# Kernel tuning notes

Measured on AMD Instinct MI355X. Metric: run time of the kernel, lower is better.

The kernel has to match this reference:

```python
import jax, jax.numpy as jnp
import numpy as np

N = 8192        # nodes
E = 131072      # random edges (16 * N); self loops appended inside reference
D = 128         # in_channels
K = int(np.ceil(0.5 * N))  # pooled nodes, ratio=0.5
NEG = 0.2       # leaky relu negative slope


def setup_inputs() -> dict:
    key = jax.random.key(0)
    ks = jax.random.split(key, 10)
    s = 0.05
    return dict(
        x=jax.random.normal(ks[0], (N, D), jnp.float32),
        edge_src=jax.random.randint(ks[1], (E,), 0, N),
        edge_off=jax.random.randint(ks[2], (E,), 0, N - 1),
        W_lin=jax.random.normal(ks[3], (D, D), jnp.float32) * s,
        b_lin=jnp.zeros((D,), jnp.float32),
        w_att=jax.random.normal(ks[4], (2 * D,), jnp.float32) * s,
        b_att=jnp.zeros((1,), jnp.float32),
        w1=jax.random.normal(ks[5], (D,), jnp.float32) * s,
        b1=jnp.zeros((1,), jnp.float32),
        w2=jax.random.normal(ks[6], (D,), jnp.float32) * s,
        w3=jax.random.normal(ks[7], (D,), jnp.float32) * s,
        b3=jnp.zeros((1,), jnp.float32),
    )


def reference(x, edge_src, edge_off, W_lin, b_lin, w_att, b_att, w1, b1, w2, w3, b3):
    # build edges with guaranteed no self loops, then add_remaining_self_loops (weight 1)
    dst = (edge_src + 1 + edge_off) % N
    loop = jnp.arange(N)
    row = jnp.concatenate([edge_src, loop])   # [Et] source j
    col = jnp.concatenate([dst, loop])        # [Et] target i
    ew = jnp.ones(row.shape, x.dtype)         # edge weights (fill_value=1)

    # GNN=None -> x_pool = x
    x_pool_j = x[row]                                             # [Et, D]
    x_q = jax.ops.segment_max(x_pool_j, col, num_segments=N)      # scatter-max at target
    x_q = (x_q @ W_lin + b_lin)[col]                              # [Et, D]

    score = jnp.concatenate([x_q, x_pool_j], axis=-1) @ w_att + b_att[0]  # [Et]
    score = jax.nn.leaky_relu(score, negative_slope=NEG)
    # edge softmax over incoming edges of each target node (stable)
    smax = jax.ops.segment_max(score, col, num_segments=N)
    e = jnp.exp(score - smax[col])
    score = e / jax.ops.segment_sum(e, col, num_segments=N)[col]
    # dropout p=0 (eval): no-op

    # attention-weighted aggregation
    x_new = jax.ops.segment_sum(x[row] * score[:, None], col, num_segments=N)  # [N, D]

    # LEConv fitness (out_channels=1): lin3(x) + sum_j w_ji * (lin1(x)_i - lin2(x)_j)
    a = x_new @ w1 + b1[0]                                        # [N]
    b = x_new @ w2                                                # [N]
    agg = jax.ops.segment_sum(ew * (a[col] - b[row]), col, num_segments=N)
    fitness = jax.nn.sigmoid(x_new @ w3 + b3[0] + agg)            # [N]

    # topk pooling (single graph): k = ceil(ratio * N)
    perm = jnp.argsort(-fitness)[:K]
    x_out = x_new[perm] * fitness[perm][:, None]                  # [K, D]

    # dense N x N attention as in original, then column-select perm
    attention = jnp.zeros((N, N), x.dtype).at[row, col].set(score)
    S_perm = attention[:, perm]                                   # [N, K] == S[:, perm]

    # A_new = S^T A S (A sparse, weight 1 per edge incl. self loops), diag removed
    T = jax.ops.segment_sum(ew[:, None] * S_perm[col], row, num_segments=N)  # A @ S_perm
    A_new = S_perm.T @ T                                          # [K, K]
    A_new = A_new * (1.0 - jnp.eye(K, dtype=x.dtype))             # remove_diag

    return x_out, A_new, perm, S_perm
```

## Files before the change

### kernel.cpp

```cpp
#include <hip/hip_runtime.h>
#include <hip/hip_bf16.h>
#include <math.h>
#include <stdint.h>

#define N_NODES 8192
#define E_EDGES 131072
#define D_DIM 128
#define M_EDGES (E_EDGES + N_NODES)
#define K_TOP 4096
#define NEG_SLOPE 0.2

__global__ void k_init_edges(const int* __restrict__ edge_src, const int* __restrict__ edge_off,
                             unsigned* __restrict__ rowA, unsigned* __restrict__ colA,
                             unsigned* __restrict__ dup,
                             unsigned* __restrict__ col_cnt, unsigned* __restrict__ row_cnt) {
    int e = blockIdx.x * blockDim.x + threadIdx.x;
    if (e >= M_EDGES) return;
    unsigned r, c;
    if (e < E_EDGES) {
        r = (unsigned)edge_src[e];
        c = (r + 1u + (unsigned)edge_off[e]) % N_NODES;
    } else {
        r = c = (unsigned)(e - E_EDGES);
    }
    rowA[e] = r; colA[e] = c; dup[e] = 0u;
    atomicAdd(&col_cnt[c], 1u);
    atomicAdd(&row_cnt[r], 1u);
}

__global__ __launch_bounds__(1024) void k_scan2(const unsigned* __restrict__ cnt0, unsigned* __restrict__ off0, unsigned* __restrict__ cur0,
                                                const unsigned* __restrict__ cnt1, unsigned* __restrict__ off1, unsigned* __restrict__ cur1) {
    const unsigned* cnt = blockIdx.x ? cnt1 : cnt0;
    unsigned* off = blockIdx.x ? off1 : off0;
    unsigned* cur = blockIdx.x ? cur1 : cur0;
    __shared__ unsigned part[1024];
    const int n = N_NODES, per = N_NODES / 1024;
    int t = threadIdx.x;
    unsigned local[8];
    unsigned s = 0;
    for (int j = 0; j < per; j++) { local[j] = cnt[t * per + j]; s += local[j]; }
    part[t] = s; __syncthreads();
    for (int d = 1; d < 1024; d <<= 1) {
        unsigned v = (t >= d) ? part[t - d] : 0u;
        __syncthreads();
        part[t] += v;
        __syncthreads();
    }
    unsigned run = (t > 0) ? part[t - 1] : 0u;
    for (int j = 0; j < per; j++) {
        off[t * per + j] = run;
        if (cur) cur[t * per + j] = run;
        run += local[j];
    }
    if (t == 1023) off[n] = run;
}

__global__ void k_fill(const unsigned* __restrict__ rowA, const unsigned* __restrict__ colA,
                       unsigned* __restrict__ col_cur, unsigned* __restrict__ row_cur,
                       unsigned* __restrict__ col_edges, unsigned* __restrict__ row_edges) {
    int e = blockIdx.x * blockDim.x + threadIdx.x;
    if (e >= M_EDGES) return;
    unsigned p1 = atomicAdd(&col_cur[colA[e]], 1u); col_edges[p1] = (unsigned)e;
    unsigned p2 = atomicAdd(&row_cur[rowA[e]], 1u); row_edges[p2] = (unsigned)e;
}

__global__ __launch_bounds__(64) void k_sortlists(unsigned* __restrict__ col_edges, const unsigned* __restrict__ col_off,
                                                  unsigned* __restrict__ row_edges, const unsigned* __restrict__ row_off,
                                                  const unsigned* __restrict__ rowA, unsigned* __restrict__ dup) {
    __shared__ unsigned buf[192];
    int node = blockIdx.x;
    int which = blockIdx.y;
    unsigned* edges = which ? row_edges : col_edges;
    const unsigned* off = which ? row_off : col_off;
    int lo = (int)off[node], hi = (int)off[node + 1];
    int n = hi - lo; if (n > 192) n = 192;
    for (int i = threadIdx.x; i < n; i += 64) buf[i] = edges[lo + i];
    __syncthreads();
    if (threadIdx.x == 0) {
        for (int i = 1; i < n; i++) {
            unsigned v = buf[i]; int j = i - 1;
            while (j >= 0 && buf[j] > v) { buf[j + 1] = buf[j]; j--; }
            buf[j + 1] = v;
        }
    }
    __syncthreads();
    for (int i = threadIdx.x; i < n; i += 64) edges[lo + i] = buf[i];
    if (which == 0) {
        for (int i = threadIdx.x; i < n; i += 64) {
            unsigned ri = rowA[buf[i]];
            bool d = false;
            for (int j = 0; j < i; j++) if (rowA[buf[j]] == ri) { d = true; break; }
            if (d) dup[buf[i]] = 1u;
        }
    }
}

__global__ __launch_bounds__(128) void k_lin(const float* __restrict__ x,
                                             const unsigned* __restrict__ col_off,
                                             const unsigned* __restrict__ col_edges,
                                             const unsigned* __restrict__ rowA,
                                             const float* __restrict__ W, const float* __restrict__ b_lin,
                                             const float* __restrict__ w_att,
                                             double* __restrict__ q_score, double* __restrict__ k_score) {
    int c = blockIdx.x, d = threadIdx.x;
    __shared__ unsigned rloc[256];
    __shared__ float xq[128];
    __shared__ double red[4];
    int lo = (int)col_off[c], hi = (int)col_off[c + 1];
    int n = hi - lo;
    for (int i = d; i < n && i < 256; i += 128) rloc[i] = rowA[col_edges[lo + i]];
    __syncthreads();
    float m = -INFINITY;
    for (int i = 0; i < n; i++) {
        unsigned r = (i < 256) ? rloc[i] : rowA[col_edges[lo + i]];
        m = fmaxf(m, x[(size_t)r * D_DIM + d]);
    }
    xq[d] = m;
    __syncthreads();
    double acc = (double)b_lin[d];
    for (int j = 0; j < 128; j++) acc += (double)xq[j] * (double)W[j * 128 + d];
    double q = acc * (double)w_att[d];
    double k = (double)x[(size_t)c * 128 + d] * (double)w_att[128 + d];
    for (int o = 32; o > 0; o >>= 1) { q += __shfl_down(q, o); k += __shfl_down(k, o); }
    if ((d & 63) == 0) { red[d >> 6] = q; red[2 + (d >> 6)] = k; }
    __syncthreads();
    if (d == 0) { q_score[c] = red[0] + red[1]; k_score[c] = red[2] + red[3]; }
}

__global__ __launch_bounds__(128) void k_sm_xnew(const float* __restrict__ x,
                                                 const unsigned* __restrict__ col_off,
                                                 const unsigned* __restrict__ col_edges,
                                                 const unsigned* __restrict__ rowA,
                                                 const double* __restrict__ q_score,
                                                 const double* __restrict__ k_score,
                                                 const float* __restrict__ b_att,
                                                 const float* __restrict__ w1, const float* __restrict__ b1,
                                                 const float* __restrict__ w2, const float* __restrict__ w3,
                                                 const float* __restrict__ b3,
                                                 double* __restrict__ score_d, float* __restrict__ score_f,
                                                 float* __restrict__ x_new, double* __restrict__ aV,
                                                 double* __restrict__ bV, double* __restrict__ finV) {
    int c = blockIdx.x, t = threadIdx.x;
    __shared__ unsigned eloc[256];
    __shared__ unsigned rloc[256];
    __shared__ double sloc[256];
    __shared__ double redd[2];
    __shared__ double red6[6];
    int lo = (int)col_off[c], hi = (int)col_off[c + 1];
    int n = hi - lo;
    for (int i = t; i < n && i < 256; i += 128) {
        unsigned e = col_edges[lo + i];
        eloc[i] = e;
        rloc[i] = rowA[e];
    }
    __syncthreads();
    double qc = q_score[c] + (double)b_att[0];
    double m = -INFINITY;
    for (int i = t; i < n; i += 128) {
        unsigned r = (i < 256) ? rloc[i] : rowA[col_edges[lo + i]];
        double s = qc + k_score[r];
        s = (s >= 0.0) ? s : NEG_SLOPE * s;
        m = fmax(m, s);
    }
    for (int o = 32; o > 0; o >>= 1) m = fmax(m, __shfl_xor(m, o));
    if ((t & 63) == 0) redd[t >> 6] = m;
    __syncthreads();
    m = fmax(redd[0], redd[1]);
    __syncthreads();
    double sum = 0.0;
    for (int i = t; i < n; i += 128) {
        unsigned r = (i < 256) ? rloc[i] : rowA[col_edges[lo + i]];
        double s = qc + k_score[r];
        s = (s >= 0.0) ? s : NEG_SLOPE * s;
        sum += exp(s - m);
    }
    for (int o = 32; o > 0; o >>= 1) sum += __shfl_xor(sum, o);
    if ((t & 63) == 0) redd[t >> 6] = sum;
    __syncthreads();
    sum = redd[0] + redd[1];
    for (int i = t; i < n; i += 128) {
        unsigned e = (i < 256) ? eloc[i] : col_edges[lo + i];
        unsigned r = (i < 256) ? rloc[i] : rowA[e];
        double s = qc + k_score[r];
        s = (s >= 0.0) ? s : NEG_SLOPE * s;
        double w = exp(s - m) / sum;
        if (i < 256) sloc[i] = w;
        score_d[e] = w;
        score_f[e] = (float)w;
    }
    __syncthreads();
    int d = t;
    double acc = 0.0;
    for (int i = 0; i < n; i++) {
        unsigned r;
        double sc;
        if (i < 256) { r = rloc[i]; sc = sloc[i]; }
        else { unsigned e = col_edges[lo + i]; r = rowA[e]; sc = score_d[e]; }
        acc += sc * (double)x[(size_t)r * 128 + d];
    }
    x_new[(size_t)c * 128 + d] = (float)acc;
    double pa = acc * (double)w1[d], pb = acc * (double)w2[d], pf = acc * (double)w3[d];
    for (int o = 32; o > 0; o >>= 1) { pa += __shfl_down(pa, o); pb += __shfl_down(pb, o); pf += __shfl_down(pf, o); }
    if ((d & 63) == 0) { int w = d >> 6; red6[w] = pa; red6[2 + w] = pb; red6[4 + w] = pf; }
    __syncthreads();
    if (d == 0) {
        aV[c] = red6[0] + red6[1] + (double)b1[0];
        bV[c] = red6[2] + red6[3];
        finV[c] = red6[4] + red6[5] + (double)b3[0];
    }
}

__global__ __launch_bounds__(64) void k_fitness(const unsigned* __restrict__ col_off,
                                                const unsigned* __restrict__ col_edges,
                                                const unsigned* __restrict__ rowA,
                                                const double* __restrict__ aV, const double* __restrict__ bV,
                                                const double* __restrict__ finV,
                                                double* __restrict__ fitness) {
    int c = blockIdx.x, t = threadIdx.x;
    int lo = (int)col_off[c], hi = (int)col_off[c + 1];
    double ac = aV[c], s = 0.0;
    for (int i = lo + t; i < hi; i += 64) s += ac - bV[rowA[col_edges[i]]];
    for (int o = 32; o > 0; o >>= 1) s += __shfl_xor(s, o);
    if (t == 0) {
        double z = finV[c] + s;
        fitness[c] = 1.0 / (1.0 + exp(-z));
    }
}

__global__ __launch_bounds__(1024) void k_sortlocal(const double* __restrict__ fitness,
                                                    unsigned long long* __restrict__ keys) {
    __shared__ unsigned long long k2[2048];
    int t = threadIdx.x, base = blockIdx.x * 2048;
    for (int i = t; i < 2048; i += 1024) {
        unsigned long long bits = (unsigned long long)__double_as_longlong(fitness[base + i]);
        unsigned long long u = (bits & 0x8000000000000000ull) ? ~bits : (bits | 0x8000000000000000ull);
        k2[i] = (~u & 0xFFFFFFFFFFFFE000ull) | (unsigned long long)(base + i);
    }
    __syncthreads();
    for (int size = 2; size <= 2048; size <<= 1) {
        for (int stride = size >> 1; stride > 0; stride >>= 1) {
            int pos = 2 * t - (t & (stride - 1));
            bool asc = ((pos & size) == 0);
            unsigned long long A = k2[pos], B = k2[pos + stride];
            if ((A > B) == asc) { k2[pos] = B; k2[pos + stride] = A; }
            __syncthreads();
        }
    }
    for (int i = t; i < 2048; i += 1024) keys[base + i] = k2[i];
}

__global__ __launch_bounds__(256) void k_merge(const unsigned long long* __restrict__ in,
                                               unsigned long long* __restrict__ out, int L) {
    int g = blockIdx.x * 256 + threadIdx.x;
    if (g >= N_NODES) return;
    int pair = g / (2 * L), r = g - pair * 2 * L;
    const unsigned long long* A = in + (size_t)pair * 2 * L;
    const unsigned long long* B = A + L;
    unsigned long long v; int p;
    if (r < L) {
        v = A[r];
        int lo = 0, hi = L;
        while (lo < hi) { int mid = (lo + hi) >> 1; if (B[mid] < v) lo = mid + 1; else hi = mid; }
        p = r + lo;
    } else {
        int j = r - L; v = B[j];
        int lo = 0, hi = L;
        while (lo < hi) { int mid = (lo + hi) >> 1; if (A[mid] < v) lo = mid + 1; else hi = mid; }
        p = j + lo;
    }
    out[(size_t)pair * 2 * L + p] = v;
}

__global__ __launch_bounds__(256) void k_merge_emit(const unsigned long long* __restrict__ in,
                                                    unsigned* __restrict__ perm_i, int* __restrict__ inv_k,
                                                    float* __restrict__ perm_out) {
    int g = blockIdx.x * 256 + threadIdx.x;
    if (g >= N_NODES) return;
    const unsigned long long* A = in;
    const unsigned long long* B = in + 4096;
    unsigned long long v; int p;
    if (g < 4096) {
        v = A[g];
        int lo = 0, hi = 4096;
        while (lo < hi) { int mid = (lo + hi) >> 1; if (B[mid] < v) lo = mid + 1; else hi = mid; }
        p = g + lo;
    } else {
        int j = g - 4096; v = B[j];
        int lo = 0, hi = 4096;
        while (lo < hi) { int mid = (lo + hi) >> 1; if (A[mid] < v) lo = mid + 1; else hi = mid; }
        p = j + lo;
    }
    unsigned idx = (unsigned)(v & 0x1FFFull);
    inv_k[idx] = (p < K_TOP) ? p : -1;
    if (p < K_TOP) { perm_i[p] = idx; perm_out[p] = (float)idx; }
}

__global__ __launch_bounds__(64) void k_scount(const unsigned* __restrict__ row_off,
                                               const unsigned* __restrict__ row_edges,
                                               const unsigned* __restrict__ colA,
                                               const unsigned* __restrict__ dup,
                                               const int* __restrict__ inv_k,
                                               unsigned* __restrict__ s_cnt) {
    int c = blockIdx.x, t = threadIdx.x;
    int lo = (int)row_off[c], hi = (int)row_off[c + 1];
    unsigned cnt = 0;
    for (int i = lo + t; i < hi; i += 64) {
        unsigned e = row_edges[i];
        if (!dup[e] && inv_k[colA[e]] >= 0) cnt++;
    }
    for (int o = 32; o > 0; o >>= 1) cnt += __shfl_xor(cnt, o);
    if (t == 0) s_cnt[c] = cnt;
}

__global__ __launch_bounds__(64) void k_sfill(const unsigned* __restrict__ row_off,
                                              const unsigned* __restrict__ row_edges,
                                              const unsigned* __restrict__ colA,
                                              const unsigned* __restrict__ dup,
                                              const int* __restrict__ inv_k,
                                              const unsigned* __restrict__ s_off,
                                              const float* __restrict__ score,
                                              unsigned* __restrict__ s_k, float* __restrict__ s_v) {
    int c = blockIdx.x, t = threadIdx.x;
    int lo = (int)row_off[c], hi = (int)row_off[c + 1];
    unsigned base = s_off[c];
    for (int i0 = lo; i0 < hi; i0 += 64) {
        int i = i0 + t;
        bool pred = false; unsigned e = 0; int kk = -1;
        if (i < hi) {
            e = row_edges[i];
            kk = inv_k[colA[e]];
            pred = (!dup[e]) && (kk >= 0);
        }
        unsigned long long mask = __ballot(pred);
        if (pred) {
            unsigned pos = (unsigned)__popcll(mask & ((1ull << t) - 1ull));
            s_k[base + pos] = (unsigned)kk;
            s_v[base + pos] = score[e];
        }
        base += (unsigned)__popcll(mask);
    }
}

__global__ __launch_bounds__(64) void k_tcount(const unsigned* __restrict__ row_off,
                                               const unsigned* __restrict__ row_edges,
                                               const unsigned* __restrict__ colA,
                                               const unsigned* __restrict__ s_cnt,
                                               unsigned* __restrict__ t_cnt) {
    int r = blockIdx.x, t = threadIdx.x;
    int lo = (int)row_off[r], hi = (int)row_off[r + 1];
    unsigned cnt = 0;
    for (int i = lo + t; i < hi; i += 64) cnt += s_cnt[colA[row_edges[i]]];
    for (int o = 32; o > 0; o >>= 1) cnt += __shfl_xor(cnt, o);
    if (t == 0) t_cnt[r] = cnt;
}

__global__ __launch_bounds__(64) void k_tfill(const unsigned* __restrict__ row_off,
                                              const unsigned* __restrict__ row_edges,
                                              const unsigned* __restrict__ colA,
                                              const unsigned* __restrict__ s_off,
                                              const unsigned* __restrict__ s_cnt,
                                              const unsigned* __restrict__ s_k,
                                              const float* __restrict__ s_v,
                                              const unsigned* __restrict__ t_off,
                                              unsigned* __restrict__ t_k, float* __restrict__ t_v,
                                              unsigned tcap) {
    int r = blockIdx.x, t = threadIdx.x;
    int lo = (int)row_off[r], hi = (int)row_off[r + 1];
    unsigned base = t_off[r];
    for (int i0 = lo; i0 < hi; i0 += 64) {
        int i = i0 + t;
        unsigned cnt = 0, c2 = 0;
        if (i < hi) { c2 = colA[row_edges[i]]; cnt = s_cnt[c2]; }
        unsigned pre = cnt;
        for (int o = 1; o < 64; o <<= 1) { unsigned v = __shfl_up(pre, o); if (t >= o) pre += v; }
        unsigned excl = pre - cnt;
        unsigned total = __shfl(pre, 63);
        if (i < hi && cnt) {
            unsigned sb = s_off[c2];
            unsigned db = base + excl;
            if (db + cnt <= tcap) {
                for (unsigned j = 0; j < cnt; j++) { t_k[db + j] = s_k[sb + j]; t_v[db + j] = s_v[sb + j]; }
            }
        }
        base += total;
    }
}

__global__ __launch_bounds__(256) void k_anew(const unsigned* __restrict__ col_off,
                                              const unsigned* __restrict__ col_edges,
                                              const unsigned* __restrict__ rowA,
                                              const unsigned* __restrict__ dup,
                                              const float* __restrict__ score,
                                              const unsigned* __restrict__ perm_i,
                                              const unsigned* __restrict__ t_off,
                                              const unsigned* __restrict__ t_k,
                                              const float* __restrict__ t_v,
                                              float* __restrict__ A_out) {
    __shared__ float acc[K_TOP];
    int k1 = blockIdx.x, t = threadIdx.x;
    for (int i = t; i < K_TOP; i += 256) acc[i] = 0.f;
    __syncthreads();
    unsigned p = perm_i[k1];
    int lo = (int)col_off[p], hi = (int)col_off[p + 1];
    for (int i = lo; i < hi; i++) {
        unsigned e = col_edges[i];
        if (dup[e]) continue;
        float sc = score[e];
        unsigned n = rowA[e];
        unsigned tb = t_off[n], te = t_off[n + 1];
        for (unsigned j = tb + t; j < te; j += 256)
            atomicAdd(&acc[t_k[j]], sc * t_v[j]);
    }
    __syncthreads();
    float* outp = &A_out[(size_t)k1 * K_TOP];
    for (int i = t; i < K_TOP; i += 256) outp[i] = (i == k1) ? 0.f : acc[i];
}

__global__ __launch_bounds__(256) void k_spermz(const unsigned* __restrict__ s_off,
                                                const unsigned* __restrict__ s_k,
                                                const float* __restrict__ s_v,
                                                float* __restrict__ S_out) {
    int r = blockIdx.x, t = threadIdx.x;
    float4* row4 = (float4*)(S_out + (size_t)r * K_TOP);
    float4 z; z.x = 0.f; z.y = 0.f; z.z = 0.f; z.w = 0.f;
    for (int i = t; i < K_TOP / 4; i += 256) row4[i] = z;
    __syncthreads();
    int lo = (int)s_off[r], hi = (int)s_off[r + 1];
    for (int j = lo + t; j < hi; j += 256)
        S_out[(size_t)r * K_TOP + s_k[j]] = s_v[j];
}

__global__ __launch_bounds__(128) void k_xout(const float* __restrict__ x_new,
                                              const double* __restrict__ fitness,
                                              const unsigned* __restrict__ perm_i,
                                              float* __restrict__ xo) {
    int k = blockIdx.x, d = threadIdx.x;
    unsigned p = perm_i[k];
    xo[(size_t)k * D_DIM + d] = x_new[(size_t)p * D_DIM + d] * (float)fitness[p];
}

extern "C" void kernel_launch(void* const* d_in, const int* in_sizes, int n_in,
                              void* d_out, int out_size, void* d_ws, size_t ws_size,
                              hipStream_t stream) {
    const float* x        = (const float*)d_in[0];
    const int*   edge_src = (const int*)d_in[1];
    const int*   edge_off = (const int*)d_in[2];
    const float* W_lin    = (const float*)d_in[3];
    const float* b_lin    = (const float*)d_in[4];
    const float* w_att    = (const float*)d_in[5];
    const float* b_att    = (const float*)d_in[6];
    const float* w1       = (const float*)d_in[7];
    const float* b1       = (const float*)d_in[8];
    const float* w2       = (const float*)d_in[9];
    const float* w3       = (const float*)d_in[10];
    const float* b3       = (const float*)d_in[11];

    float* out = (float*)d_out;
    float* out_xout  = out;
    float* out_anew  = out + (size_t)K_TOP * D_DIM;
    float* out_perm  = out_anew + (size_t)K_TOP * K_TOP;
    float* out_sperm = out_perm + K_TOP;

    char* wp = (char*)d_ws;
    char* wend = wp + ws_size;
    auto alloc = [&](size_t bytes) -> void* {
        void* p = (void*)wp;
        wp += (bytes + 255) & ~(size_t)255;
        return p;
    };
    unsigned* rowA      = (unsigned*)alloc((size_t)M_EDGES * 4);
    unsigned* colA      = (unsigned*)alloc((size_t)M_EDGES * 4);
    unsigned* dup       = (unsigned*)alloc((size_t)M_EDGES * 4);
    double*   score_d   = (double*)alloc((size_t)M_EDGES * 8);
    float*    score     = (float*)alloc((size_t)M_EDGES * 4);
    unsigned* cnts      = (unsigned*)alloc((size_t)2 * N_NODES * 4);
    unsigned* col_cnt   = cnts;
    unsigned* row_cnt   = cnts + N_NODES;
    unsigned* col_off   = (unsigned*)alloc((size_t)(N_NODES + 1) * 4);
    unsigned* row_off   = (unsigned*)alloc((size_t)(N_NODES + 1) * 4);
    unsigned* col_cur   = (unsigned*)alloc((size_t)N_NODES * 4);
    unsigned* row_cur   = (unsigned*)alloc((size_t)N_NODES * 4);
    unsigned* col_edges = (unsigned*)alloc((size_t)M_EDGES * 4);
    unsigned* row_edges = (unsigned*)alloc((size_t)M_EDGES * 4);
    float*    x_new     = (float*)alloc((size_t)N_NODES * D_DIM * 4);
    double*   q_score   = (double*)alloc((size_t)N_NODES * 8);
    double*   k_score   = (double*)alloc((size_t)N_NODES * 8);
    double*   aV        = (double*)alloc((size_t)N_NODES * 8);
    double*   bV        = (double*)alloc((size_t)N_NODES * 8);
    double*   finV      = (double*)alloc((size_t)N_NODES * 8);
    double*   fitness   = (double*)alloc((size_t)N_NODES * 8);
    unsigned long long* keys_a = (unsigned long long*)alloc((size_t)N_NODES * 8);
    unsigned long long* keys_b = (unsigned long long*)alloc((size_t)N_NODES * 8);
    unsigned* perm_i    = (unsigned*)alloc((size_t)K_TOP * 4);
    int*      inv_k     = (int*)alloc((size_t)N_NODES * 4);
    unsigned* s_cnt     = (unsigned*)alloc((size_t)N_NODES * 4);
    unsigned* s_off     = (unsigned*)alloc((size_t)(N_NODES + 1) * 4);
    unsigned* s_k       = (unsigned*)alloc((size_t)M_EDGES * 4);
    float*    s_v       = (float*)alloc((size_t)M_EDGES * 4);
    unsigned* t_cnt     = (unsigned*)alloc((size_t)N_NODES * 4);
    unsigned* t_off     = (unsigned*)alloc((size_t)(N_NODES + 1) * 4);
    size_t remain = (size_t)(wend - wp);
    size_t tcap = remain / 8;
    if (tcap > (size_t)6 * 1024 * 1024) tcap = (size_t)6 * 1024 * 1024;
    unsigned* t_k = (unsigned*)alloc(tcap * 4);
    float*    t_v = (float*)alloc(tcap * 4);

    hipMemsetAsync(cnts, 0, (size_t)2 * N_NODES * 4, stream);

    k_init_edges<<<(M_EDGES + 255) / 256, 256, 0, stream>>>(edge_src, edge_off, rowA, colA, dup, col_cnt, row_cnt);
    k_scan2<<<2, 1024, 0, stream>>>(col_cnt, col_off, col_cur, row_cnt, row_off, row_cur);
    k_fill<<<(M_EDGES + 255) / 256, 256, 0, stream>>>(rowA, colA, col_cur, row_cur, col_edges, row_edges);
    k_sortlists<<<dim3(N_NODES, 2), 64, 0, stream>>>(col_edges, col_off, row_edges, row_off, rowA, dup);
    k_lin<<<N_NODES, 128, 0, stream>>>(x, col_off, col_edges, rowA, W_lin, b_lin, w_att, q_score, k_score);
    k_sm_xnew<<<N_NODES, 128, 0, stream>>>(x, col_off, col_edges, rowA, q_score, k_score, b_att,
                                           w1, b1, w2, w3, b3, score_d, score, x_new, aV, bV, finV);
    k_fitness<<<N_NODES, 64, 0, stream>>>(col_off, col_edges, rowA, aV, bV, finV, fitness);
    k_sortlocal<<<4, 1024, 0, stream>>>(fitness, keys_a);
    k_merge<<<N_NODES / 256, 256, 0, stream>>>(keys_a, keys_b, 2048);
    k_merge_emit<<<N_NODES / 256, 256, 0, stream>>>(keys_b, perm_i, inv_k, out_perm);
    k_scount<<<N_NODES, 64, 0, stream>>>(row_off, row_edges, colA, dup, inv_k, s_cnt);
    k_tcount<<<N_NODES, 64, 0, stream>>>(row_off, row_edges, colA, s_cnt, t_cnt);
    k_scan2<<<2, 1024, 0, stream>>>(s_cnt, s_off, (unsigned*)nullptr, t_cnt, t_off, (unsigned*)nullptr);
    k_sfill<<<N_NODES, 64, 0, stream>>>(row_off, row_edges, colA, dup, inv_k, s_off, score, s_k, s_v);
    k_tfill<<<N_NODES, 64, 0, stream>>>(row_off, row_edges, colA, s_off, s_cnt, s_k, s_v, t_off,
                                        t_k, t_v, (unsigned)tcap);
    k_spermz<<<N_NODES, 256, 0, stream>>>(s_off, s_k, s_v, out_sperm);
    k_anew<<<K_TOP, 256, 0, stream>>>(col_off, col_edges, rowA, dup, score, perm_i, t_off, t_k, t_v, out_anew);
    k_xout<<<K_TOP, 128, 0, stream>>>(x_new, fitness, perm_i, out_xout);
}
```

Baseline: 304.4 us.

## Fuse output kernels, drop list sorting, compute A_new by two-hop traversal

Removes the per-node insertion sort and moves duplicate-edge detection into the linear kernel, which now handles 16 nodes per block with W staged in LDS. Fitness computation is folded into the local bitonic sort kernel. The S_perm count/fill and T materialisation passes are replaced by one fused launch. That launch writes S_perm rows, builds A_new by walking two hops of the row CSR with LDS atomics, and emits x_out. This cuts many launches and intermediate buffers, but the A_new blocks do more irregular gather work, and the linear kernel has fewer blocks and does a quadratic duplicate check in global memory.

New measurement: 732.1 us. +140.5%, slower.

```diff
diff --git a/kernel.cpp b/kernel.cpp
--- a/kernel.cpp
+++ b/kernel.cpp
@@ -64,67 +64,50 @@
     unsigned p2 = atomicAdd(&row_cur[rowA[e]], 1u); row_edges[p2] = (unsigned)e;
 }
 
-__global__ __launch_bounds__(64) void k_sortlists(unsigned* __restrict__ col_edges, const unsigned* __restrict__ col_off,
-                                                  unsigned* __restrict__ row_edges, const unsigned* __restrict__ row_off,
-                                                  const unsigned* __restrict__ rowA, unsigned* __restrict__ dup) {
-    __shared__ unsigned buf[192];
-    int node = blockIdx.x;
-    int which = blockIdx.y;
-    unsigned* edges = which ? row_edges : col_edges;
-    const unsigned* off = which ? row_off : col_off;
-    int lo = (int)off[node], hi = (int)off[node + 1];
-    int n = hi - lo; if (n > 192) n = 192;
-    for (int i = threadIdx.x; i < n; i += 64) buf[i] = edges[lo + i];
-    __syncthreads();
-    if (threadIdx.x == 0) {
-        for (int i = 1; i < n; i++) {
-            unsigned v = buf[i]; int j = i - 1;
-            while (j >= 0 && buf[j] > v) { buf[j + 1] = buf[j]; j--; }
-            buf[j + 1] = v;
-        }
-    }
-    __syncthreads();
-    for (int i = threadIdx.x; i < n; i += 64) edges[lo + i] = buf[i];
-    if (which == 0) {
-        for (int i = threadIdx.x; i < n; i += 64) {
-            unsigned ri = rowA[buf[i]];
-            bool d = false;
-            for (int j = 0; j < i; j++) if (rowA[buf[j]] == ri) { d = true; break; }
-            if (d) dup[buf[i]] = 1u;
-        }
-    }
-}
-
 __global__ __launch_bounds__(128) void k_lin(const float* __restrict__ x,
                                              const unsigned* __restrict__ col_off,
                                              const unsigned* __restrict__ col_edges,
                                              const unsigned* __restrict__ rowA,
+                                             unsigned* __restrict__ dup,
                                              const float* __restrict__ W, const float* __restrict__ b_lin,
                                              const float* __restrict__ w_att,
                                              double* __restrict__ q_score, double* __restrict__ k_score) {
-    int c = blockIdx.x, d = threadIdx.x;
-    __shared__ unsigned rloc[256];
-    __shared__ float xq[128];
+    __shared__ float Wlds[D_DIM * D_DIM];
+    __shared__ float xq[D_DIM];
     __shared__ double red[4];
-    int lo = (int)col_off[c], hi = (int)col_off[c + 1];
-    int n = hi - lo;
-    for (int i = d; i < n && i < 256; i += 128) rloc[i] = rowA[col_edges[lo + i]];
-    __syncthreads();
-    float m = -INFINITY;
-    for (int i = 0; i < n; i++) {
-        unsigned r = (i < 256) ? rloc[i] : rowA[col_edges[lo + i]];
-        m = fmaxf(m, x[(size_t)r * D_DIM + d]);
-    }
-    xq[d] = m;
-    __syncthreads();
-    double acc = (double)b_lin[d];
-    for (int j = 0; j < 128; j++) acc += (double)xq[j] * (double)W[j * 128 + d];
-    double q = acc * (double)w_att[d];
-    double k = (double)x[(size_t)c * 128 + d] * (double)w_att[128 + d];
-    for (int o = 32; o > 0; o >>= 1) { q += __shfl_down(q, o); k += __shfl_down(k, o); }
-    if ((d & 63) == 0) { red[d >> 6] = q; red[2 + (d >> 6)] = k; }
-    __syncthreads();
-    if (d == 0) { q_score[c] = red[0] + red[1]; k_score[c] = red[2] + red[3]; }
+    int t = threadIdx.x;
+    for (int idx = t; idx < D_DIM * D_DIM; idx += 128) Wlds[idx] = W[idx];
+    double bl = (double)b_lin[t];
+    double wq = (double)w_att[t];
+    double wk = (double)w_att[D_DIM + t];
+    __syncthreads();
+    for (int nb = 0; nb < 16; nb++) {
+        int c = blockIdx.x * 16 + nb;
+        int lo = (int)col_off[c], hi = (int)col_off[c + 1];
+        int n = hi - lo;
+        for (int i = t; i < n; i += 128) {
+            unsigned ri = rowA[col_edges[lo + i]];
+            for (int j = 0; j < i; j++) {
+                if (rowA[col_edges[lo + j]] == ri) { dup[col_edges[lo + i]] = 1u; break; }
+            }
+        }
+        float m = -INFINITY;
+        for (int i = 0; i < n; i++) {
+            unsigned r = rowA[col_edges[lo + i]];
+            m = fmaxf(m, x[(size_t)r * D_DIM + t]);
+        }
+        xq[t] = m;
+        __syncthreads();
+        double acc = bl;
+        for (int j = 0; j < D_DIM; j++) acc += (double)xq[j] * (double)Wlds[j * D_DIM + t];
+        double q = acc * wq;
+        double k = (double)x[(size_t)c * D_DIM + t] * wk;
+        for (int o = 32; o > 0; o >>= 1) { q += __shfl_down(q, o); k += __shfl_down(k, o); }
+        if ((t & 63) == 0) { red[t >> 6] = q; red[2 + (t >> 6)] = k; }
+        __syncthreads();
+        if (t == 0) { q_score[c] = red[0] + red[1]; k_score[c] = red[2] + red[3]; }
+        __syncthreads();
+    }
 }
 
 __global__ __launch_bounds__(128) void k_sm_xnew(const float* __restrict__ x,
@@ -196,9 +179,9 @@
         double sc;
         if (i < 256) { r = rloc[i]; sc = sloc[i]; }
         else { unsigned e = col_edges[lo + i]; r = rowA[e]; sc = score_d[e]; }
-        acc += sc * (double)x[(size_t)r * 128 + d];
-    }
-    x_new[(size_t)c * 128 + d] = (float)acc;
+        acc += sc * (double)x[(size_t)r * D_DIM + d];
+    }
+    x_new[(size_t)c * D_DIM + d] = (float)acc;
     double pa = acc * (double)w1[d], pb = acc * (double)w2[d], pf = acc * (double)w3[d];
     for (int o = 32; o > 0; o >>= 1) { pa += __shfl_down(pa, o); pb += __shfl_down(pb, o); pf += __shfl_down(pf, o); }
     if ((d & 63) == 0) { int w = d >> 6; red6[w] = pa; red6[2 + w] = pb; red6[4 + w] = pf; }
@@ -210,31 +193,25 @@
     }
 }
 
-__global__ __launch_bounds__(64) void k_fitness(const unsigned* __restrict__ col_off,
-                                                const unsigned* __restrict__ col_edges,
-                                                const unsigned* __restrict__ rowA,
-                                                const double* __restrict__ aV, const double* __restrict__ bV,
-                                                const double* __restrict__ finV,
-                                                double* __restrict__ fitness) {
-    int c = blockIdx.x, t = threadIdx.x;
-    int lo = (int)col_off[c], hi = (int)col_off[c + 1];
-    double ac = aV[c], s = 0.0;
-    for (int i = lo + t; i < hi; i += 64) s += ac - bV[rowA[col_edges[i]]];
-    for (int o = 32; o > 0; o >>= 1) s += __shfl_xor(s, o);
-    if (t == 0) {
-        double z = finV[c] + s;
-        fitness[c] = 1.0 / (1.0 + exp(-z));
-    }
-}
-
-__global__ __launch_bounds__(1024) void k_sortlocal(const double* __restrict__ fitness,
-                                                    unsigned long long* __restrict__ keys) {
+__global__ __launch_bounds__(1024) void k_sortfit(const unsigned* __restrict__ col_off,
+                                                  const unsigned* __restrict__ col_edges,
+                                                  const unsigned* __restrict__ rowA,
+                                                  const double* __restrict__ aV, const double* __restrict__ bV,
+                                                  const double* __restrict__ finV,
+                                                  double* __restrict__ fitness,
+                                                  unsigned long long* __restrict__ keys) {
     __shared__ unsigned long long k2[2048];
     int t = threadIdx.x, base = blockIdx.x * 2048;
-    for (int i = t; i < 2048; i += 1024) {
-        unsigned long long bits = (unsigned long long)__double_as_longlong(fitness[base + i]);
-        unsigned long long u = (bits & 0x8000000000000000ull) ? ~bits : (bits | 0x8000000000000000ull);
-        k2[i] = (~u & 0xFFFFFFFFFFFFE000ull) | (unsigned long long)(base + i);
+    for (int u = 0; u < 2; u++) {
+        int c = base + u * 1024 + t;
+        int lo = (int)col_off[c], hi = (int)col_off[c + 1];
+        double s = finV[c] + (double)(hi - lo) * aV[c];
+        for (int i = lo; i < hi; i++) s -= bV[rowA[col_edges[i]]];
+        double fit = 1.0 / (1.0 + exp(-s));
+        fitness[c] = fit;
+        unsigned long long bits = (unsigned long long)__double_as_longlong(fit);
+        unsigned long long uo = (bits & 0x8000000000000000ull) ? ~bits : (bits | 0x8000000000000000ull);
+        k2[u * 1024 + t] = (~uo & 0xFFFFFFFFFFFFE000ull) | (unsigned long long)c;
     }
     __syncthreads();
     for (int size = 2; size <= 2048; size <<= 1) {
@@ -295,148 +272,82 @@
     if (p < K_TOP) { perm_i[p] = idx; perm_out[p] = (float)idx; }
 }
 
-__global__ __launch_bounds__(64) void k_scount(const unsigned* __restrict__ row_off,
-                                               const unsigned* __restrict__ row_edges,
-                                               const unsigned* __restrict__ colA,
-                                               const unsigned* __restrict__ dup,
-                                               const int* __restrict__ inv_k,
-                                               unsigned* __restrict__ s_cnt) {
-    int c = blockIdx.x, t = threadIdx.x;
-    int lo = (int)row_off[c], hi = (int)row_off[c + 1];
-    unsigned cnt = 0;
-    for (int i = lo + t; i < hi; i += 64) {
-        unsigned e = row_edges[i];
-        if (!dup[e] && inv_k[colA[e]] >= 0) cnt++;
-    }
-    for (int o = 32; o > 0; o >>= 1) cnt += __shfl_xor(cnt, o);
-    if (t == 0) s_cnt[c] = cnt;
-}
-
-__global__ __launch_bounds__(64) void k_sfill(const unsigned* __restrict__ row_off,
-                                              const unsigned* __restrict__ row_edges,
-                                              const unsigned* __restrict__ colA,
-                                              const unsigned* __restrict__ dup,
-                                              const int* __restrict__ inv_k,
-                                              const unsigned* __restrict__ s_off,
-                                              const float* __restrict__ score,
-                                              unsigned* __restrict__ s_k, float* __restrict__ s_v) {
-    int c = blockIdx.x, t = threadIdx.x;
-    int lo = (int)row_off[c], hi = (int)row_off[c + 1];
-    unsigned base = s_off[c];
-    for (int i0 = lo; i0 < hi; i0 += 64) {
-        int i = i0 + t;
-        bool pred = false; unsigned e = 0; int kk = -1;
-        if (i < hi) {
-            e = row_edges[i];
-            kk = inv_k[colA[e]];
-            pred = (!dup[e]) && (kk >= 0);
-        }
-        unsigned long long mask = __ballot(pred);
-        if (pred) {
-            unsigned pos = (unsigned)__popcll(mask & ((1ull << t) - 1ull));
-            s_k[base + pos] = (unsigned)kk;
-            s_v[base + pos] = score[e];
-        }
-        base += (unsigned)__popcll(mask);
-    }
-}
-
-__global__ __launch_bounds__(64) void k_tcount(const unsigned* __restrict__ row_off,
-                                               const unsigned* __restrict__ row_edges,
-                                               const unsigned* __restrict__ colA,
-                                               const unsigned* __restrict__ s_cnt,
-                                               unsigned* __restrict__ t_cnt) {
-    int r = blockIdx.x, t = threadIdx.x;
-    int lo = (int)row_off[r], hi = (int)row_off[r + 1];
-    unsigned cnt = 0;
-    for (int i = lo + t; i < hi; i += 64) cnt += s_cnt[colA[row_edges[i]]];
-    for (int o = 32; o > 0; o >>= 1) cnt += __shfl_xor(cnt, o);
-    if (t == 0) t_cnt[r] = cnt;
-}
-
-__global__ __launch_bounds__(64) void k_tfill(const unsigned* __restrict__ row_off,
-                                              const unsigned* __restrict__ row_edges,
-                                              const unsigned* __restrict__ colA,
-                                              const unsigned* __restrict__ s_off,
-                                              const unsigned* __restrict__ s_cnt,
-                                              const unsigned* __restrict__ s_k,
-                                              const float* __restrict__ s_v,
-                                              const unsigned* __restrict__ t_off,
-                                              unsigned* __restrict__ t_k, float* __restrict__ t_v,
-                                              unsigned tcap) {
-    int r = blockIdx.x, t = threadIdx.x;
-    int lo = (int)row_off[r], hi = (int)row_off[r + 1];
-    unsigned base = t_off[r];
-    for (int i0 = lo; i0 < hi; i0 += 64) {
-        int i = i0 + t;
-        unsigned cnt = 0, c2 = 0;
-        if (i < hi) { c2 = colA[row_edges[i]]; cnt = s_cnt[c2]; }
-        unsigned pre = cnt;
-        for (int o = 1; o < 64; o <<= 1) { unsigned v = __shfl_up(pre, o); if (t >= o) pre += v; }
-        unsigned excl = pre - cnt;
-        unsigned total = __shfl(pre, 63);
-        if (i < hi && cnt) {
-            unsigned sb = s_off[c2];
-            unsigned db = base + excl;
-            if (db + cnt <= tcap) {
-                for (unsigned j = 0; j < cnt; j++) { t_k[db + j] = s_k[sb + j]; t_v[db + j] = s_v[sb + j]; }
+__global__ __launch_bounds__(256) void k_fused_out(const unsigned* __restrict__ col_off,
+                                                   const unsigned* __restrict__ col_edges,
+                                                   const unsigned* __restrict__ row_off,
+                                                   const unsigned* __restrict__ row_edges,
+                                                   const unsigned* __restrict__ rowA,
+                                                   const unsigned* __restrict__ colA,
+                                                   const unsigned* __restrict__ dup,
+                                                   const float* __restrict__ score,
+                                                   const int* __restrict__ inv_k,
+                                                   const unsigned* __restrict__ perm_i,
+                                                   const float* __restrict__ x_new,
+                                                   const double* __restrict__ fitness,
+                                                   float* __restrict__ S_out,
+                                                   float* __restrict__ A_out,
+                                                   float* __restrict__ xo) {
+    __shared__ float acc[K_TOP];
+    __shared__ unsigned nloc[64];
+    __shared__ float scloc[64];
+    int bid = blockIdx.x, t = threadIdx.x;
+    if (bid < N_NODES) {
+        int r = bid;
+        float4* row4 = (float4*)(S_out + (size_t)r * K_TOP);
+        float4 z; z.x = 0.f; z.y = 0.f; z.z = 0.f; z.w = 0.f;
+        for (int i = t; i < K_TOP / 4; i += 256) row4[i] = z;
+        __syncthreads();
+        int lo = (int)row_off[r], hi = (int)row_off[r + 1];
+        for (int j = lo + t; j < hi; j += 256) {
+            unsigned e = row_edges[j];
+            if (!dup[e]) {
+                int kk = inv_k[colA[e]];
+                if (kk >= 0) S_out[(size_t)r * K_TOP + kk] = score[e];
             }
         }
-        base += total;
-    }
-}
-
-__global__ __launch_bounds__(256) void k_anew(const unsigned* __restrict__ col_off,
-                                              const unsigned* __restrict__ col_edges,
-                                              const unsigned* __restrict__ rowA,
-                                              const unsigned* __restrict__ dup,
-                                              const float* __restrict__ score,
-                                              const unsigned* __restrict__ perm_i,
-                                              const unsigned* __restrict__ t_off,
-                                              const unsigned* __restrict__ t_k,
-                                              const float* __restrict__ t_v,
-                                              float* __restrict__ A_out) {
-    __shared__ float acc[K_TOP];
-    int k1 = blockIdx.x, t = threadIdx.x;
-    for (int i = t; i < K_TOP; i += 256) acc[i] = 0.f;
-    __syncthreads();
-    unsigned p = perm_i[k1];
-    int lo = (int)col_off[p], hi = (int)col_off[p + 1];
-    for (int i = lo; i < hi; i++) {
-        unsigned e = col_edges[i];
-        if (dup[e]) continue;
-        float sc = score[e];
-        unsigned n = rowA[e];
-        unsigned tb = t_off[n], te = t_off[n + 1];
-        for (unsigned j = tb + t; j < te; j += 256)
-            atomicAdd(&acc[t_k[j]], sc * t_v[j]);
-    }
-    __syncthreads();
-    float* outp = &A_out[(size_t)k1 * K_TOP];
-    for (int i = t; i < K_TOP; i += 256) outp[i] = (i == k1) ? 0.f : acc[i];
-}
-
-__global__ __launch_bounds__(256) void k_spermz(const unsigned* __restrict__ s_off,
-                                                const unsigned* __restrict__ s_k,
-                                                const float* __restrict__ s_v,
-                                                float* __restrict__ S_out) {
-    int r = blockIdx.x, t = threadIdx.x;
-    float4* row4 = (float4*)(S_out + (size_t)r * K_TOP);
-    float4 z; z.x = 0.f; z.y = 0.f; z.z = 0.f; z.w = 0.f;
-    for (int i = t; i < K_TOP / 4; i += 256) row4[i] = z;
-    __syncthreads();
-    int lo = (int)s_off[r], hi = (int)s_off[r + 1];
-    for (int j = lo + t; j < hi; j += 256)
-        S_out[(size_t)r * K_TOP + s_k[j]] = s_v[j];
-}
-
-__global__ __launch_bounds__(128) void k_xout(const float* __restrict__ x_new,
-                                              const double* __restrict__ fitness,
-                                              const unsigned* __restrict__ perm_i,
-                                              float* __restrict__ xo) {
-    int k = blockIdx.x, d = threadIdx.x;
-    unsigned p = perm_i[k];
-    xo[(size_t)k * D_DIM + d] = x_new[(size_t)p * D_DIM + d] * (float)fitness[p];
+    } else if (bid < N_NODES + K_TOP) {
+        int k1 = bid - N_NODES;
+        for (int i = t; i < K_TOP; i += 256) acc[i] = 0.f;
+        unsigned p = perm_i[k1];
+        int lo = (int)col_off[p], hi = (int)col_off[p + 1];
+        for (int c0 = lo; c0 < hi; c0 += 64) {
+            int nin = hi - c0; if (nin > 64) nin = 64;
+            __syncthreads();
+            if (t < nin) {
+                unsigned e = col_edges[c0 + t];
+                nloc[t] = dup[e] ? 0xFFFFFFFFu : rowA[e];
+                scloc[t] = score[e];
+            }
+            __syncthreads();
+            int g = t >> 3, lane = t & 7;
+            for (int i = g; i < nin; i += 32) {
+                unsigned n = nloc[i];
+                if (n == 0xFFFFFFFFu) continue;
+                float sc = scloc[i];
+                int rlo = (int)row_off[n], rhi = (int)row_off[n + 1];
+                for (int j = rlo + lane; j < rhi; j += 8) {
+                    unsigned c2 = colA[row_edges[j]];
+                    int qlo = (int)row_off[c2], qhi = (int)row_off[c2 + 1];
+                    for (int q = qlo; q < qhi; q++) {
+                        unsigned e3 = row_edges[q];
+                        if (dup[e3]) continue;
+                        int kk = inv_k[colA[e3]];
+                        if (kk >= 0) atomicAdd(&acc[kk], sc * score[e3]);
+                    }
+                }
+            }
+        }
+        __syncthreads();
+        float* outp = &A_out[(size_t)k1 * K_TOP];
+        for (int i = t; i < K_TOP; i += 256) outp[i] = (i == k1) ? 0.f : acc[i];
+    } else {
+        int gid = (bid - N_NODES - K_TOP) * 256 + t;
+        for (int u = gid; u < K_TOP * D_DIM; u += 32 * 256) {
+            int k = u >> 7, d = u & 127;
+            unsigned pp = perm_i[k];
+            xo[u] = x_new[(size_t)pp * D_DIM + d] * (float)fitness[pp];
+        }
+    }
 }
 
 extern "C" void kernel_launch(void* const* d_in, const int* in_sizes, int n_in,
@@ -462,7 +373,6 @@
     float* out_sperm = out_perm + K_TOP;
 
     char* wp = (char*)d_ws;
-    char* wend = wp + ws_size;
     auto alloc = [&](size_t bytes) -> void* {
         void* p = (void*)wp;
         wp += (bytes + 255) & ~(size_t)255;
@@ -493,38 +403,19 @@
     unsigned long long* keys_b = (unsigned long long*)alloc((size_t)N_NODES * 8);
     unsigned* perm_i    = (unsigned*)alloc((size_t)K_TOP * 4);
     int*      inv_k     = (int*)alloc((size_t)N_NODES * 4);
-    unsigned* s_cnt     = (unsigned*)alloc((size_t)N_NODES * 4);
-    unsigned* s_off     = (unsigned*)alloc((size_t)(N_NODES + 1) * 4);
-    unsigned* s_k       = (unsigned*)alloc((size_t)M_EDGES * 4);
-    float*    s_v       = (float*)alloc((size_t)M_EDGES * 4);
-    unsigned* t_cnt     = (unsigned*)alloc((size_t)N_NODES * 4);
-    unsigned* t_off     = (unsigned*)alloc((size_t)(N_NODES + 1) * 4);
-    size_t remain = (size_t)(wend - wp);
-    size_t tcap = remain / 8;
-    if (tcap > (size_t)6 * 1024 * 1024) tcap = (size_t)6 * 1024 * 1024;
-    unsigned* t_k = (unsigned*)alloc(tcap * 4);
-    float*    t_v = (float*)alloc(tcap * 4);
 
     hipMemsetAsync(cnts, 0, (size_t)2 * N_NODES * 4, stream);
 
     k_init_edges<<<(M_EDGES + 255) / 256, 256, 0, stream>>>(edge_src, edge_off, rowA, colA, dup, col_cnt, row_cnt);
     k_scan2<<<2, 1024, 0, stream>>>(col_cnt, col_off, col_cur, row_cnt, row_off, row_cur);
     k_fill<<<(M_EDGES + 255) / 256, 256, 0, stream>>>(rowA, colA, col_cur, row_cur, col_edges, row_edges);
-    k_sortlists<<<dim3(N_NODES, 2), 64, 0, stream>>>(col_edges, col_off, row_edges, row_off, rowA, dup);
-    k_lin<<<N_NODES, 128, 0, stream>>>(x, col_off, col_edges, rowA, W_lin, b_lin, w_att, q_score, k_score);
+    k_lin<<<N_NODES / 16, 128, 0, stream>>>(x, col_off, col_edges, rowA, dup, W_lin, b_lin, w_att, q_score, k_score);
     k_sm_xnew<<<N_NODES, 128, 0, stream>>>(x, col_off, col_edges, rowA, q_score, k_score, b_att,
                                            w1, b1, w2, w3, b3, score_d, score, x_new, aV, bV, finV);
-    k_fitness<<<N_NODES, 64, 0, stream>>>(col_off, col_edges, rowA, aV, bV, finV, fitness);
-    k_sortlocal<<<4, 1024, 0, stream>>>(fitness, keys_a);
+    k_sortfit<<<4, 1024, 0, stream>>>(col_off, col_edges, rowA, aV, bV, finV, fitness, keys_a);
     k_merge<<<N_NODES / 256, 256, 0, stream>>>(keys_a, keys_b, 2048);
     k_merge_emit<<<N_NODES / 256, 256, 0, stream>>>(keys_b, perm_i, inv_k, out_perm);
-    k_scount<<<N_NODES, 64, 0, stream>>>(row_off, row_edges, colA, dup, inv_k, s_cnt);
-    k_tcount<<<N_NODES, 64, 0, stream>>>(row_off, row_edges, colA, s_cnt, t_cnt);
-    k_scan2<<<2, 1024, 0, stream>>>(s_cnt, s_off, (unsigned*)nullptr, t_cnt, t_off, (unsigned*)nullptr);
-    k_sfill<<<N_NODES, 64, 0, stream>>>(row_off, row_edges, colA, dup, inv_k, s_off, score, s_k, s_v);
-    k_tfill<<<N_NODES, 64, 0, stream>>>(row_off, row_edges, colA, s_off, s_cnt, s_k, s_v, t_off,
-                                        t_k, t_v, (unsigned)tcap);
-    k_spermz<<<N_NODES, 256, 0, stream>>>(s_off, s_k, s_v, out_sperm);
-    k_anew<<<K_TOP, 256, 0, stream>>>(col_off, col_edges, rowA, dup, score, perm_i, t_off, t_k, t_v, out_anew);
-    k_xout<<<K_TOP, 128, 0, stream>>>(x_new, fitness, perm_i, out_xout);
-}
+    k_fused_out<<<N_NODES + K_TOP + 32, 256, 0, stream>>>(col_off, col_edges, row_off, row_edges,
+                                                          rowA, colA, dup, score, inv_k, perm_i,
+                                                          x_new, fitness, out_sperm, out_anew, out_xout);
+}
```

## Drop per-node list sorting, fold dup detection into k_lin, fuse output kernels

Applied to the files above, without the earlier changes.

Removes the k_sortlists kernel, which sorted every node's in- and out-edge lists with a single-thread insertion sort. Duplicate-edge detection moves into k_lin as a quadratic check over each node's unsorted incoming list. The fitness computation is folded into the block-local bitonic sort kernel. The S_perm, A_new and x_out writers become one launch that branches on block index. This saves the sort pass and several launches, but the per-node edge order now follows atomic fill order, so which duplicate gets flagged and the floating-point summation order are no longer deterministic. The fitness pass also now runs on only 4 blocks.

New measurement: 340.6 us. 11.9% more time.

```diff
diff --git a/kernel.cpp b/kernel.cpp
--- a/kernel.cpp
+++ b/kernel.cpp
@@ -64,67 +64,44 @@
     unsigned p2 = atomicAdd(&row_cur[rowA[e]], 1u); row_edges[p2] = (unsigned)e;
 }
 
-__global__ __launch_bounds__(64) void k_sortlists(unsigned* __restrict__ col_edges, const unsigned* __restrict__ col_off,
-                                                  unsigned* __restrict__ row_edges, const unsigned* __restrict__ row_off,
-                                                  const unsigned* __restrict__ rowA, unsigned* __restrict__ dup) {
-    __shared__ unsigned buf[192];
-    int node = blockIdx.x;
-    int which = blockIdx.y;
-    unsigned* edges = which ? row_edges : col_edges;
-    const unsigned* off = which ? row_off : col_off;
-    int lo = (int)off[node], hi = (int)off[node + 1];
-    int n = hi - lo; if (n > 192) n = 192;
-    for (int i = threadIdx.x; i < n; i += 64) buf[i] = edges[lo + i];
-    __syncthreads();
-    if (threadIdx.x == 0) {
-        for (int i = 1; i < n; i++) {
-            unsigned v = buf[i]; int j = i - 1;
-            while (j >= 0 && buf[j] > v) { buf[j + 1] = buf[j]; j--; }
-            buf[j + 1] = v;
-        }
-    }
-    __syncthreads();
-    for (int i = threadIdx.x; i < n; i += 64) edges[lo + i] = buf[i];
-    if (which == 0) {
-        for (int i = threadIdx.x; i < n; i += 64) {
-            unsigned ri = rowA[buf[i]];
-            bool d = false;
-            for (int j = 0; j < i; j++) if (rowA[buf[j]] == ri) { d = true; break; }
-            if (d) dup[buf[i]] = 1u;
-        }
-    }
-}
-
 __global__ __launch_bounds__(128) void k_lin(const float* __restrict__ x,
                                              const unsigned* __restrict__ col_off,
                                              const unsigned* __restrict__ col_edges,
                                              const unsigned* __restrict__ rowA,
+                                             unsigned* __restrict__ dup,
                                              const float* __restrict__ W, const float* __restrict__ b_lin,
                                              const float* __restrict__ w_att,
                                              double* __restrict__ q_score, double* __restrict__ k_score) {
-    int c = blockIdx.x, d = threadIdx.x;
+    int c = blockIdx.x, t = threadIdx.x;
     __shared__ unsigned rloc[256];
     __shared__ float xq[128];
     __shared__ double red[4];
     int lo = (int)col_off[c], hi = (int)col_off[c + 1];
     int n = hi - lo;
-    for (int i = d; i < n && i < 256; i += 128) rloc[i] = rowA[col_edges[lo + i]];
-    __syncthreads();
+    for (int i = t; i < n && i < 256; i += 128) rloc[i] = rowA[col_edges[lo + i]];
+    __syncthreads();
+    for (int i = t; i < n; i += 128) {
+        unsigned ri = (i < 256) ? rloc[i] : rowA[col_edges[lo + i]];
+        for (int j = 0; j < i; j++) {
+            unsigned rj = (j < 256) ? rloc[j] : rowA[col_edges[lo + j]];
+            if (rj == ri) { dup[col_edges[lo + i]] = 1u; break; }
+        }
+    }
     float m = -INFINITY;
     for (int i = 0; i < n; i++) {
         unsigned r = (i < 256) ? rloc[i] : rowA[col_edges[lo + i]];
-        m = fmaxf(m, x[(size_t)r * D_DIM + d]);
-    }
-    xq[d] = m;
-    __syncthreads();
-    double acc = (double)b_lin[d];
-    for (int j = 0; j < 128; j++) acc += (double)xq[j] * (double)W[j * 128 + d];
-    double q = acc * (double)w_att[d];
-    double k = (double)x[(size_t)c * 128 + d] * (double)w_att[128 + d];
+        m = fmaxf(m, x[(size_t)r * D_DIM + t]);
+    }
+    xq[t] = m;
+    __syncthreads();
+    double acc = (double)b_lin[t];
+    for (int j = 0; j < D_DIM; j++) acc += (double)xq[j] * (double)W[j * D_DIM + t];
+    double q = acc * (double)w_att[t];
+    double k = (double)x[(size_t)c * D_DIM + t] * (double)w_att[D_DIM + t];
     for (int o = 32; o > 0; o >>= 1) { q += __shfl_down(q, o); k += __shfl_down(k, o); }
-    if ((d & 63) == 0) { red[d >> 6] = q; red[2 + (d >> 6)] = k; }
-    __syncthreads();
-    if (d == 0) { q_score[c] = red[0] + red[1]; k_score[c] = red[2] + red[3]; }
+    if ((t & 63) == 0) { red[t >> 6] = q; red[2 + (t >> 6)] = k; }
+    __syncthreads();
+    if (t == 0) { q_score[c] = red[0] + red[1]; k_score[c] = red[2] + red[3]; }
 }
 
 __global__ __launch_bounds__(128) void k_sm_xnew(const float* __restrict__ x,
@@ -196,9 +173,9 @@
         double sc;
         if (i < 256) { r = rloc[i]; sc = sloc[i]; }
         else { unsigned e = col_edges[lo + i]; r = rowA[e]; sc = score_d[e]; }
-        acc += sc * (double)x[(size_t)r * 128 + d];
-    }
-    x_new[(size_t)c * 128 + d] = (float)acc;
+        acc += sc * (double)x[(size_t)r * D_DIM + d];
+    }
+    x_new[(size_t)c * D_DIM + d] = (float)acc;
     double pa = acc * (double)w1[d], pb = acc * (double)w2[d], pf = acc * (double)w3[d];
     for (int o = 32; o > 0; o >>= 1) { pa += __shfl_down(pa, o); pb += __shfl_down(pb, o); pf += __shfl_down(pf, o); }
     if ((d & 63) == 0) { int w = d >> 6; red6[w] = pa; red6[2 + w] = pb; red6[4 + w] = pf; }
@@ -210,31 +187,25 @@
     }
 }
 
-__global__ __launch_bounds__(64) void k_fitness(const unsigned* __restrict__ col_off,
-                                                const unsigned* __restrict__ col_edges,
-                                                const unsigned* __restrict__ rowA,
-                                                const double* __restrict__ aV, const double* __restrict__ bV,
-                                                const double* __restrict__ finV,
-                                                double* __restrict__ fitness) {
-    int c = blockIdx.x, t = threadIdx.x;
-    int lo = (int)col_off[c], hi = (int)col_off[c + 1];
-    double ac = aV[c], s = 0.0;
-    for (int i = lo + t; i < hi; i += 64) s += ac - bV[rowA[col_edges[i]]];
-    for (int o = 32; o > 0; o >>= 1) s += __shfl_xor(s, o);
-    if (t == 0) {
-        double z = finV[c] + s;
-        fitness[c] = 1.0 / (1.0 + exp(-z));
-    }
-}
-
-__global__ __launch_bounds__(1024) void k_sortlocal(const double* __restrict__ fitness,
-                                                    unsigned long long* __restrict__ keys) {
+__global__ __launch_bounds__(1024) void k_sortfit(const unsigned* __restrict__ col_off,
+                                                  const unsigned* __restrict__ col_edges,
+                                                  const unsigned* __restrict__ rowA,
+                                                  const double* __restrict__ aV, const double* __restrict__ bV,
+                                                  const double* __restrict__ finV,
+                                                  double* __restrict__ fitness,
+                                                  unsigned long long* __restrict__ keys) {
     __shared__ unsigned long long k2[2048];
     int t = threadIdx.x, base = blockIdx.x * 2048;
-    for (int i = t; i < 2048; i += 1024) {
-        unsigned long long bits = (unsigned long long)__double_as_longlong(fitness[base + i]);
-        unsigned long long u = (bits & 0x8000000000000000ull) ? ~bits : (bits | 0x8000000000000000ull);
-        k2[i] = (~u & 0xFFFFFFFFFFFFE000ull) | (unsigned long long)(base + i);
+    for (int u = 0; u < 2; u++) {
+        int c = base + u * 1024 + t;
+        int lo = (int)col_off[c], hi = (int)col_off[c + 1];
+        double s = finV[c] + (double)(hi - lo) * aV[c];
+        for (int i = lo; i < hi; i++) s -= bV[rowA[col_edges[i]]];
+        double fit = 1.0 / (1.0 + exp(-s));
+        fitness[c] = fit;
+        unsigned long long bits = (unsigned long long)__double_as_longlong(fit);
+        unsigned long long uo = (bits & 0x8000000000000000ull) ? ~bits : (bits | 0x8000000000000000ull);
+        k2[u * 1024 + t] = (~uo & 0xFFFFFFFFFFFFE000ull) | (unsigned long long)c;
     }
     __syncthreads();
     for (int size = 2; size <= 2048; size <<= 1) {
@@ -386,57 +357,66 @@
     }
 }
 
-__global__ __launch_bounds__(256) void k_anew(const unsigned* __restrict__ col_off,
-                                              const unsigned* __restrict__ col_edges,
-                                              const unsigned* __restrict__ rowA,
-                                              const unsigned* __restrict__ dup,
-                                              const float* __restrict__ score,
-                                              const unsigned* __restrict__ perm_i,
-                                              const unsigned* __restrict__ t_off,
-                                              const unsigned* __restrict__ t_k,
-                                              const float* __restrict__ t_v,
-                                              float* __restrict__ A_out) {
+__global__ __launch_bounds__(256) void k_fused_out(const unsigned* __restrict__ col_off,
+                                                   const unsigned* __restrict__ col_edges,
+                                                   const unsigned* __restrict__ row_off,
+                                                   const unsigned* __restrict__ row_edges,
+                                                   const unsigned* __restrict__ rowA,
+                                                   const unsigned* __restrict__ colA,
+                                                   const unsigned* __restrict__ dup,
+                                                   const float* __restrict__ score,
+                                                   const int* __restrict__ inv_k,
+                                                   const unsigned* __restrict__ perm_i,
+                                                   const unsigned* __restrict__ t_off,
+                                                   const unsigned* __restrict__ t_k,
+                                                   const float* __restrict__ t_v,
+                                                   const float* __restrict__ x_new,
+                                                   const double* __restrict__ fitness,
+                                                   float* __restrict__ S_out,
+                                                   float* __restrict__ A_out,
+                                                   float* __restrict__ xo) {
     __shared__ float acc[K_TOP];
-    int k1 = blockIdx.x, t = threadIdx.x;
-    for (int i = t; i < K_TOP; i += 256) acc[i] = 0.f;
-    __syncthreads();
-    unsigned p = perm_i[k1];
-    int lo = (int)col_off[p], hi = (int)col_off[p + 1];
-    for (int i = lo; i < hi; i++) {
-        unsigned e = col_edges[i];
-        if (dup[e]) continue;
-        float sc = score[e];
-        unsigned n = rowA[e];
-        unsigned tb = t_off[n], te = t_off[n + 1];
-        for (unsigned j = tb + t; j < te; j += 256)
-            atomicAdd(&acc[t_k[j]], sc * t_v[j]);
-    }
-    __syncthreads();
-    float* outp = &A_out[(size_t)k1 * K_TOP];
-    for (int i = t; i < K_TOP; i += 256) outp[i] = (i == k1) ? 0.f : acc[i];
-}
-
-__global__ __launch_bounds__(256) void k_spermz(const unsigned* __restrict__ s_off,
-                                                const unsigned* __restrict__ s_k,
-                                                const float* __restrict__ s_v,
-                                                float* __restrict__ S_out) {
-    int r = blockIdx.x, t = threadIdx.x;
-    float4* row4 = (float4*)(S_out + (size_t)r * K_TOP);
-    float4 z; z.x = 0.f; z.y = 0.f; z.z = 0.f; z.w = 0.f;
-    for (int i = t; i < K_TOP / 4; i += 256) row4[i] = z;
-    __syncthreads();
-    int lo = (int)s_off[r], hi = (int)s_off[r + 1];
-    for (int j = lo + t; j < hi; j += 256)
-        S_out[(size_t)r * K_TOP + s_k[j]] = s_v[j];
-}
-
-__global__ __launch_bounds__(128) void k_xout(const float* __restrict__ x_new,
-                                              const double* __restrict__ fitness,
-                                              const unsigned* __restrict__ perm_i,
-                                              float* __restrict__ xo) {
-    int k = blockIdx.x, d = threadIdx.x;
-    unsigned p = perm_i[k];
-    xo[(size_t)k * D_DIM + d] = x_new[(size_t)p * D_DIM + d] * (float)fitness[p];
+    int bid = blockIdx.x, t = threadIdx.x;
+    if (bid < N_NODES) {
+        int r = bid;
+        float4* row4 = (float4*)(S_out + (size_t)r * K_TOP);
+        float4 z; z.x = 0.f; z.y = 0.f; z.z = 0.f; z.w = 0.f;
+        for (int i = t; i < K_TOP / 4; i += 256) row4[i] = z;
+        __syncthreads();
+        int lo = (int)row_off[r], hi = (int)row_off[r + 1];
+        for (int j = lo + t; j < hi; j += 256) {
+            unsigned e = row_edges[j];
+            if (!dup[e]) {
+                int kk = inv_k[colA[e]];
+                if (kk >= 0) S_out[(size_t)r * K_TOP + kk] = score[e];
+            }
+        }
+    } else if (bid < N_NODES + K_TOP) {
+        int k1 = bid - N_NODES;
+        for (int i = t; i < K_TOP; i += 256) acc[i] = 0.f;
+        __syncthreads();
+        unsigned p = perm_i[k1];
+        int lo = (int)col_off[p], hi = (int)col_off[p + 1];
+        for (int i = lo; i < hi; i++) {
+            unsigned e = col_edges[i];
+            if (dup[e]) continue;
+            float sc = score[e];
+            unsigned n = rowA[e];
+            unsigned tb = t_off[n], te = t_off[n + 1];
+            for (unsigned j = tb + t; j < te; j += 256)
+                atomicAdd(&acc[t_k[j]], sc * t_v[j]);
+        }
+        __syncthreads();
+        float* outp = &A_out[(size_t)k1 * K_TOP];
+        for (int i = t; i < K_TOP; i += 256) outp[i] = (i == k1) ? 0.f : acc[i];
+    } else {
+        int gid = (bid - N_NODES - K_TOP) * 256 + t;
+        for (int u = gid; u < K_TOP * D_DIM; u += 32 * 256) {
+            int k = u >> 7, d = u & 127;
+            unsigned pp = perm_i[k];
+            xo[u] = x_new[(size_t)pp * D_DIM + d] * (float)fitness[pp];
+        }
+    }
 }
 
 extern "C" void kernel_launch(void* const* d_in, const int* in_sizes, int n_in,
@@ -510,12 +490,10 @@
     k_init_edges<<<(M_EDGES + 255) / 256, 256, 0, stream>>>(edge_src, edge_off, rowA, colA, dup, col_cnt, row_cnt);
     k_scan2<<<2, 1024, 0, stream>>>(col_cnt, col_off, col_cur, row_cnt, row_off, row_cur);
     k_fill<<<(M_EDGES + 255) / 256, 256, 0, stream>>>(rowA, colA, col_cur, row_cur, col_edges, row_edges);
-    k_sortlists<<<dim3(N_NODES, 2), 64, 0, stream>>>(col_edges, col_off, row_edges, row_off, rowA, dup);
-    k_lin<<<N_NODES, 128, 0, stream>>>(x, col_off, col_edges, rowA, W_lin, b_lin, w_att, q_score, k_score);
+    k_lin<<<N_NODES, 128, 0, stream>>>(x, col_off, col_edges, rowA, dup, W_lin, b_lin, w_att, q_score, k_score);
     k_sm_xnew<<<N_NODES, 128, 0, stream>>>(x, col_off, col_edges, rowA, q_score, k_score, b_att,
                                            w1, b1, w2, w3, b3, score_d, score, x_new, aV, bV, finV);
-    k_fitness<<<N_NODES, 64, 0, stream>>>(col_off, col_edges, rowA, aV, bV, finV, fitness);
-    k_sortlocal<<<4, 1024, 0, stream>>>(fitness, keys_a);
+    k_sortfit<<<4, 1024, 0, stream>>>(col_off, col_edges, rowA, aV, bV, finV, fitness, keys_a);
     k_merge<<<N_NODES / 256, 256, 0, stream>>>(keys_a, keys_b, 2048);
     k_merge_emit<<<N_NODES / 256, 256, 0, stream>>>(keys_b, perm_i, inv_k, out_perm);
     k_scount<<<N_NODES, 64, 0, stream>>>(row_off, row_edges, colA, dup, inv_k, s_cnt);
@@ -524,7 +502,8 @@
     k_sfill<<<N_NODES, 64, 0, stream>>>(row_off, row_edges, colA, dup, inv_k, s_off, score, s_k, s_v);
     k_tfill<<<N_NODES, 64, 0, stream>>>(row_off, row_edges, colA, s_off, s_cnt, s_k, s_v, t_off,
                                         t_k, t_v, (unsigned)tcap);
-    k_spermz<<<N_NODES, 256, 0, stream>>>(s_off, s_k, s_v, out_sperm);
-    k_anew<<<K_TOP, 256, 0, stream>>>(col_off, col_edges, rowA, dup, score, perm_i, t_off, t_k, t_v, out_anew);
-    k_xout<<<K_TOP, 128, 0, stream>>>(x_new, fitness, perm_i, out_xout);
-}
+    k_fused_out<<<N_NODES + K_TOP + 32, 256, 0, stream>>>(col_off, col_edges, row_off, row_edges,
+                                                          rowA, colA, dup, score, inv_k, perm_i,
+                                                          t_off, t_k, t_v, x_new, fitness,
+                                                          out_sperm, out_anew, out_xout);
+}
```
